# Optimization experiments

Measured on AMD Instinct MI355X. Metric: run time of the kernel, lower is better.

The kernel has to match this reference:

```python
import jax, jax.numpy as jnp
import numpy as np

N = 131072  # time steps
D = 4       # SDE state dimension


def setup_inputs() -> dict:
    key = jax.random.key(0)
    k = jax.random.split(key, 6)
    F = 0.1 * jax.random.normal(k[0], (D, D), jnp.float32)  # only shape/dtype used by filter
    H = jnp.zeros((1, D), jnp.float32).at[0, 0].set(1.0)    # observe first state component
    P_inf = jnp.eye(D, dtype=jnp.float32)
    # stable per-step transitions: spectral radius ~0.9
    A_seq = 0.9 * jnp.eye(D, dtype=jnp.float32)[None] + 0.02 * jax.random.normal(k[1], (N, D, D), jnp.float32)
    # PSD process noise per step
    S = 0.05 * jax.random.normal(k[2], (N, D, D), jnp.float32)
    Q_seq = jnp.einsum('nij,nkj->nik', S, S) + 1e-3 * jnp.eye(D, dtype=jnp.float32)[None]
    residual = jax.random.normal(k[3], (N,), jnp.float32)   # y - mean_fn(times)
    mask = jnp.ones((N,), jnp.float32)                      # all steps observed
    R_seq = 0.1 + 0.05 * jax.random.uniform(k[4], (N,), jnp.float32)  # noise_var + floor
    return dict(F=F, H=H, P_inf=P_inf, A_seq=A_seq, Q_seq=Q_seq,
                residual=residual, mask=mask, R_seq=R_seq)


def _kalman_filter(F, H, P_inf, A_seq, Q_seq, residual, mask, R_seq):
    d = F.shape[0]
    eye = jnp.eye(d, dtype=F.dtype)
    h = H[0]  # (d,)
    log_2pi = jnp.log(2.0 * jnp.pi).astype(F.dtype)

    def step(carry, inputs):
        m, P = carry
        A, Q, r_n, mask_n, R_n = inputs
        m_pred = A @ m
        P_pred = A @ P @ A.T + Q
        P_pred = 0.5 * (P_pred + P_pred.T)
        Ph = P_pred @ h                 # (d,)
        S = h @ Ph + R_n                # innovation variance
        innov = r_n - h @ m_pred
        is_obs = mask_n == 1
        S_safe = jnp.where(is_obs, S, 1.0)
        K = jnp.where(is_obs, Ph / S_safe, jnp.zeros_like(Ph))
        m_new = m_pred + K * innov
        I_KH = eye - K[:, None] * h[None, :]
        P_new = I_KH @ P_pred @ I_KH.T + R_n * (K[:, None] * K[None, :])
        P_new = 0.5 * (P_new + P_new.T)
        ll = jnp.where(is_obs, -0.5 * (log_2pi + jnp.log(S_safe) + innov * innov / S_safe), 0.0)
        return (m_new, P_new), (m_pred, P_pred, m_new, P_new, ll)

    m0 = jnp.zeros(d, dtype=F.dtype)
    _, (m_pred_seq, P_pred_seq, m_filt_seq, P_filt_seq, ll_seq) = jax.lax.scan(
        step, (m0, P_inf), (A_seq, Q_seq, residual, mask, R_seq))
    return m_pred_seq, P_pred_seq, m_filt_seq, P_filt_seq, jnp.sum(ll_seq)


def _rts_smoother(m_pred_seq, P_pred_seq, m_filt_seq, P_filt_seq, A_seq):
    def step(carry, inputs):
        m_ns, P_ns = carry
        m_f, P_f, m_pn, P_pn, A_n = inputs
        J = jnp.linalg.solve(P_pn.T, A_n @ P_f.T).T
        m_s = m_f + J @ (m_ns - m_pn)
        P_s = P_f + J @ (P_ns - P_pn) @ J.T
        P_s = 0.5 * (P_s + P_s.T)
        return (m_s, P_s), (m_s, P_s)

    m_T = m_filt_seq[-1]
    P_T = P_filt_seq[-1]
    inputs = (m_filt_seq[:-1], P_filt_seq[:-1], m_pred_seq[1:], P_pred_seq[1:], A_seq[1:])
    _, (m_s, P_s) = jax.lax.scan(step, (m_T, P_T), inputs, reverse=True)
    return (jnp.concatenate([m_s, m_T[None]], axis=0),
            jnp.concatenate([P_s, P_T[None]], axis=0))


def reference(F, H, P_inf, A_seq, Q_seq, residual, mask, R_seq):
    m_pred, P_pred, m_filt, P_filt, log_marginal = _kalman_filter(
        F, H, P_inf, A_seq, Q_seq, residual, mask, R_seq)
    m_smooth, P_smooth = _rts_smoother(m_pred, P_pred, m_filt, P_filt, A_seq)
    h = H[0]
    means = m_smooth @ h                                   # (N,) observation-space means
    vars_ = jnp.einsum('i,nij,j->n', h, P_smooth, h)       # (N,) marginal variances
    return means, vars_, log_marginal
```

## Files before the change

kernel.cpp:

```cpp
#include <hip/hip_runtime.h>
#include <math.h>

#define NN 131072
#define WUP 48
#define TPB 256
#define NBLK (NN / TPB)
#define WINF (TPB + WUP + 1)
#define WINB (TPB + WUP - 1)
#define LOG2PI 1.8378770664093453f

typedef __attribute__((ext_vector_type(2))) float f2;

__device__ float4 g_f[5][NN];
__device__ float4 g_J[4][NN];
__device__ float4 g_W[4][NN];
__device__ float4 g_u[NN];
__device__ double g_llb[NBLK];

__device__ __forceinline__ f2 bc(float s) {
  f2 r = {s, s};
  return r;
}
#define PF(a, b, c) __builtin_elementwise_fma((a), (b), (c))

template <int E>
__device__ __forceinline__ void ldpk(const float4 (*s)[E], int w, f2* M) {
#pragma unroll
  for (int c = 0; c < 4; ++c) {
    float4 v = s[c][w];
    M[2 * c] = f2{v.x, v.y};
    M[2 * c + 1] = f2{v.z, v.w};
  }
}

__device__ __forceinline__ void kf_step_pk(const f2* __restrict__ AT, const f2* __restrict__ Q,
                                           float r, float mk, float R, f2* __restrict__ m,
                                           f2* __restrict__ P, float& Ss, float& innov,
                                           bool& obs) {
  float m0 = m[0][0], m1 = m[0][1], m2_ = m[1][0], m3 = m[1][1];
  f2 mp[2];
#pragma unroll
  for (int p = 0; p < 2; ++p) {
    f2 acc = AT[p] * bc(m0);
    acc = PF(bc(m1), AT[2 + p], acc);
    acc = PF(bc(m2_), AT[4 + p], acc);
    acc = PF(bc(m3), AT[6 + p], acc);
    mp[p] = acc;
  }

  f2 T[8];
#pragma unroll
  for (int i = 0; i < 4; ++i) {
    float a0 = AT[0 + (i >> 1)][i & 1];
    float a1 = AT[2 + (i >> 1)][i & 1];
    float a2 = AT[4 + (i >> 1)][i & 1];
    float a3 = AT[6 + (i >> 1)][i & 1];
#pragma unroll
    for (int p = 0; p < 2; ++p) {
      f2 acc = P[p] * bc(a0);
      acc = PF(bc(a1), P[2 + p], acc);
      acc = PF(bc(a2), P[4 + p], acc);
      acc = PF(bc(a3), P[6 + p], acc);
      T[2 * i + p] = acc;
    }
  }

  f2 Pp[8];
#pragma unroll
  for (int i = 0; i < 4; ++i) {
    float t0 = T[2 * i][0], t1 = T[2 * i][1], t2 = T[2 * i + 1][0], t3 = T[2 * i + 1][1];
#pragma unroll
    for (int p = 0; p < 2; ++p) {
      f2 acc = PF(bc(t0), AT[p], Q[2 * i + p]);
      acc = PF(bc(t1), AT[2 + p], acc);
      acc = PF(bc(t2), AT[4 + p], acc);
      acc = PF(bc(t3), AT[6 + p], acc);
      Pp[2 * i + p] = acc;
    }
  }

  float S = Pp[0][0] + R;
  innov = r - mp[0][0];
  obs = (mk == 1.0f);
  Ss = obs ? S : 1.0f;
  float kf = obs ? (1.0f / Ss) : 0.0f;
  f2 K[2] = {Pp[0] * bc(kf), Pp[1] * bc(kf)};
#pragma unroll
  for (int p = 0; p < 2; ++p) m[p] = PF(K[p], bc(innov), mp[p]);

#pragma unroll
  for (int i = 0; i < 4; ++i) {
    float Ki = K[i >> 1][i & 1];
#pragma unroll
    for (int p = 0; p < 2; ++p) P[2 * i + p] = PF(bc(-Ki), Pp[p], Pp[2 * i + p]);
  }
}

__device__ __forceinline__ void chol_solve_pk(const f2* __restrict__ S, const f2* __restrict__ T,
                                              f2* __restrict__ X) {
  float s00 = S[0][0];
  float s10 = S[2][0], s11 = S[2][1];
  float s20 = S[4][0], s21 = S[4][1], s22 = S[5][0];
  float s30 = S[6][0], s31 = S[6][1], s32 = S[7][0], s33 = S[7][1];
  float l00 = sqrtf(s00), i00 = 1.f / l00;
  float l10 = s10 * i00, l20 = s20 * i00, l30 = s30 * i00;
  float l11 = sqrtf(s11 - l10 * l10), i11 = 1.f / l11;
  float l21 = (s21 - l20 * l10) * i11;
  float l31 = (s31 - l30 * l10) * i11;
  float l22 = sqrtf(s22 - l20 * l20 - l21 * l21), i22 = 1.f / l22;
  float l32 = (s32 - l30 * l20 - l31 * l21) * i22;
  float l33 = sqrtf(s33 - l30 * l30 - l31 * l31 - l32 * l32), i33 = 1.f / l33;
#pragma unroll
  for (int c = 0; c < 4; ++c) {
    float t0 = T[0 + (c >> 1)][c & 1];
    float t1 = T[2 + (c >> 1)][c & 1];
    float t2 = T[4 + (c >> 1)][c & 1];
    float t3 = T[6 + (c >> 1)][c & 1];
    float y0 = t0 * i00;
    float y1 = (t1 - l10 * y0) * i11;
    float y2 = (t2 - l20 * y0 - l21 * y1) * i22;
    float y3 = (t3 - l30 * y0 - l31 * y1 - l32 * y2) * i33;
    float x3 = y3 * i33;
    float x2 = (y2 - l32 * x3) * i22;
    float x1 = (y1 - l21 * x2 - l31 * x3) * i11;
    float x0 = (y0 - l10 * x1 - l20 * x2 - l30 * x3) * i00;
    X[0 + (c >> 1)][c & 1] = x0;
    X[2 + (c >> 1)][c & 1] = x1;
    X[4 + (c >> 1)][c & 1] = x2;
    X[6 + (c >> 1)][c & 1] = x3;
  }
}

__device__ __forceinline__ void make_record_pk(int n, const f2* __restrict__ m,
                                               const f2* __restrict__ P,
                                               const f2* __restrict__ AT,
                                               const f2* __restrict__ Q) {
  float m0 = m[0][0], m1 = m[0][1], m2_ = m[1][0], m3 = m[1][1];
  f2 pm[2];
#pragma unroll
  for (int p = 0; p < 2; ++p) {
    f2 acc = AT[p] * bc(m0);
    acc = PF(bc(m1), AT[2 + p], acc);
    acc = PF(bc(m2_), AT[4 + p], acc);
    acc = PF(bc(m3), AT[6 + p], acc);
    pm[p] = acc;
  }

  f2 T[8];
#pragma unroll
  for (int i = 0; i < 4; ++i) {
    float a0 = AT[0 + (i >> 1)][i & 1];
    float a1 = AT[2 + (i >> 1)][i & 1];
    float a2 = AT[4 + (i >> 1)][i & 1];
    float a3 = AT[6 + (i >> 1)][i & 1];
#pragma unroll
    for (int p = 0; p < 2; ++p) {
      f2 acc = P[p] * bc(a0);
      acc = PF(bc(a1), P[2 + p], acc);
      acc = PF(bc(a2), P[4 + p], acc);
      acc = PF(bc(a3), P[6 + p], acc);
      T[2 * i + p] = acc;
    }
  }

  f2 Ppn[8];
#pragma unroll
  for (int i = 0; i < 4; ++i) {
    float t0 = T[2 * i][0], t1 = T[2 * i][1], t2 = T[2 * i + 1][0], t3 = T[2 * i + 1][1];
#pragma unroll
    for (int p = 0; p < 2; ++p) {
      f2 acc = PF(bc(t0), AT[p], Q[2 * i + p]);
      acc = PF(bc(t1), AT[2 + p], acc);
      acc = PF(bc(t2), AT[4 + p], acc);
      acc = PF(bc(t3), AT[6 + p], acc);
      Ppn[2 * i + p] = acc;
    }
  }

  f2 X[8];
  chol_solve_pk(Ppn, T, X);

  float p0 = pm[0][0], p1 = pm[0][1], p2 = pm[1][0], p3 = pm[1][1];
  f2 u[2];
#pragma unroll
  for (int p = 0; p < 2; ++p) {
    f2 acc = X[p] * bc(p0);
    acc = PF(bc(p1), X[2 + p], acc);
    acc = PF(bc(p2), X[4 + p], acc);
    acc = PF(bc(p3), X[6 + p], acc);
    u[p] = m[p] - acc;
  }

  f2 Jp[8];
#pragma unroll
  for (int i = 0; i < 4; ++i) {
    float x0 = X[0 + (i >> 1)][i & 1];
    float x1 = X[2 + (i >> 1)][i & 1];
    float x2 = X[4 + (i >> 1)][i & 1];
    float x3 = X[6 + (i >> 1)][i & 1];
#pragma unroll
    for (int p = 0; p < 2; ++p) {
      f2 acc = Ppn[p] * bc(x0);
      acc = PF(bc(x1), Ppn[2 + p], acc);
      acc = PF(bc(x2), Ppn[4 + p], acc);
      acc = PF(bc(x3), Ppn[6 + p], acc);
      Jp[2 * i + p] = acc;
    }
  }
  f2 W[8];
#pragma unroll
  for (int i = 0; i < 4; ++i) {
    float j0 = Jp[2 * i][0], j1 = Jp[2 * i][1], j2 = Jp[2 * i + 1][0], j3 = Jp[2 * i + 1][1];
#pragma unroll
    for (int p = 0; p < 2; ++p) {
      f2 acc = X[p] * bc(j0);
      acc = PF(bc(j1), X[2 + p], acc);
      acc = PF(bc(j2), X[4 + p], acc);
      acc = PF(bc(j3), X[6 + p], acc);
      W[2 * i + p] = P[2 * i + p] - acc;
    }
  }

#pragma unroll
  for (int i = 0; i < 4; ++i)
    g_J[i][n] = make_float4(X[2 * i][0], X[2 * i][1], X[2 * i + 1][0], X[2 * i + 1][1]);
#pragma unroll
  for (int i = 0; i < 4; ++i)
    g_W[i][n] = make_float4(W[2 * i][0], W[2 * i][1], W[2 * i + 1][0], W[2 * i + 1][1]);
  g_u[n] = make_float4(u[0][0], u[0][1], u[1][0], u[1][1]);
}

__device__ __forceinline__ void rts_affine_pk(const f2* __restrict__ X, const f2* __restrict__ W,
                                              const f2* __restrict__ u, f2* __restrict__ ms,
                                              f2* __restrict__ Ps) {
  float s0 = ms[0][0], s1 = ms[0][1], s2 = ms[1][0], s3 = ms[1][1];
  f2 nms[2];
#pragma unroll
  for (int p = 0; p < 2; ++p) {
    f2 acc = PF(bc(s0), X[p], u[p]);
    acc = PF(bc(s1), X[2 + p], acc);
    acc = PF(bc(s2), X[4 + p], acc);
    acc = PF(bc(s3), X[6 + p], acc);
    nms[p] = acc;
  }
  f2 V[8];
#pragma unroll
  for (int i = 0; i < 4; ++i) {
    float x0 = X[0 + (i >> 1)][i & 1];
    float x1 = X[2 + (i >> 1)][i & 1];
    float x2 = X[4 + (i >> 1)][i & 1];
    float x3 = X[6 + (i >> 1)][i & 1];
#pragma unroll
    for (int p = 0; p < 2; ++p) {
      f2 acc = Ps[p] * bc(x0);
      acc = PF(bc(x1), Ps[2 + p], acc);
      acc = PF(bc(x2), Ps[4 + p], acc);
      acc = PF(bc(x3), Ps[6 + p], acc);
      V[2 * i + p] = acc;
    }
  }
#pragma unroll
  for (int i = 0; i < 4; ++i) {
    float v0 = V[2 * i][0], v1 = V[2 * i][1], v2 = V[2 * i + 1][0], v3 = V[2 * i + 1][1];
#pragma unroll
    for (int p = 0; p < 2; ++p) {
      f2 acc = PF(bc(v0), X[p], W[2 * i + p]);
      acc = PF(bc(v1), X[2 + p], acc);
      acc = PF(bc(v2), X[4 + p], acc);
      acc = PF(bc(v3), X[6 + p], acc);
      Ps[2 * i + p] = acc;
    }
  }
  ms[0] = nms[0];
  ms[1] = nms[1];
}

__global__ __launch_bounds__(TPB, 1) void fwd_kernel(const float* __restrict__ P_inf,
                                                     const float* __restrict__ A_seq,
                                                     const float* __restrict__ Q_seq,
                                                     const float* __restrict__ residual,
                                                     const float* __restrict__ mask,
                                                     const float* __restrict__ R_seq) {
  __shared__ float4 sAT[4][WINF], sQ[4][WINF];
  __shared__ float sr[WINF], smk[WINF], sR[WINF];
  __shared__ double sh[TPB];

  const int B = blockIdx.x * TPB;
  const int base = B - WUP;
  const float4* Af4 = (const float4*)A_seq;
  const float4* Qf4 = (const float4*)Q_seq;
  for (int f = threadIdx.x; f < WINF * 4; f += TPB) {
    int w = f >> 2, c = f & 3;
    int k = base + w;
    k = k < 0 ? 0 : (k > NN - 1 ? NN - 1 : k);
    float4 row = Af4[(size_t)k * 4 + c];
    ((float*)&sAT[0][w])[c] = row.x;
    ((float*)&sAT[1][w])[c] = row.y;
    ((float*)&sAT[2][w])[c] = row.z;
    ((float*)&sAT[3][w])[c] = row.w;
    sQ[c][w] = Qf4[(size_t)k * 4 + c];
  }
  for (int w = threadIdx.x; w < WINF; w += TPB) {
    int k = base + w;
    k = k < 0 ? 0 : (k > NN - 1 ? NN - 1 : k);
    sr[w] = residual[k];
    smk[w] = mask[k];
    sR[w] = R_seq[k];
  }
  __syncthreads();

  const int t = threadIdx.x;
  const int n = B + t;
  int s0 = n - WUP;
  if (s0 < 0) s0 = 0;

  f2 m[2] = {f2{0.f, 0.f}, f2{0.f, 0.f}};
  f2 P[8];
#pragma unroll
  for (int i = 0; i < 4; ++i) {
    P[2 * i] = f2{P_inf[i * 4 + 0], P_inf[i * 4 + 1]};
    P[2 * i + 1] = f2{P_inf[i * 4 + 2], P_inf[i * 4 + 3]};
  }

  float Ss = 1.f, innov = 0.f;
  bool obs = false;
  for (int k = s0; k <= n; ++k) {
    int w = k - base;
    f2 AT[8], Q[8];
    ldpk<WINF>(sAT, w, AT);
    ldpk<WINF>(sQ, w, Q);
    kf_step_pk(AT, Q, sr[w], smk[w], sR[w], m, P, Ss, innov, obs);
  }

#pragma unroll
  for (int c = 0; c < 4; ++c)
    g_f[c][n] = make_float4(P[2 * c][0], P[2 * c][1], P[2 * c + 1][0], P[2 * c + 1][1]);
  g_f[4][n] = make_float4(m[0][0], m[0][1], m[1][0], m[1][1]);

  if (n < NN - 1) {
    int w = n + 1 - base;
    f2 AT[8], Q[8];
    ldpk<WINF>(sAT, w, AT);
    ldpk<WINF>(sQ, w, Q);
    make_record_pk(n, m, P, AT, Q);
  }

  sh[t] = obs ? (double)(-0.5f * (LOG2PI + logf(Ss) + innov * innov / Ss)) : 0.0;
  __syncthreads();
#pragma unroll
  for (int w = TPB / 2; w > 0; w >>= 1) {
    if (t < w) sh[t] += sh[t + w];
    __syncthreads();
  }
  if (t == 0) g_llb[blockIdx.x] = sh[0];
}

__global__ __launch_bounds__(TPB, 1) void bwd_kernel(float* __restrict__ out) {
  __shared__ float4 sX[4][WINB], sW[4][WINB];
  __shared__ float4 su[WINB];
  __shared__ double shd[TPB];

  const int B = blockIdx.x * TPB;
  const int t = threadIdx.x;
  const int n = B + t;
  int e = n + WUP;
  if (e > NN - 1) e = NN - 1;

  f2 ms[2], Ps[8];
#pragma unroll
  for (int c = 0; c < 4; ++c) {
    float4 v = g_f[c][e];
    Ps[2 * c] = f2{v.x, v.y};
    Ps[2 * c + 1] = f2{v.z, v.w};
  }
  {
    float4 v = g_f[4][e];
    ms[0] = f2{v.x, v.y};
    ms[1] = f2{v.z, v.w};
  }

  for (int f = t; f < WINB * 4; f += TPB) {
    int w = f >> 2, c = f & 3;
    int k = B + w;
    if (k > NN - 1) k = NN - 1;
    sX[c][w] = g_J[c][k];
    sW[c][w] = g_W[c][k];
  }
  for (int w = t; w < WINB; w += TPB) {
    int k = B + w;
    if (k > NN - 1) k = NN - 1;
    su[w] = g_u[k];
  }
  __syncthreads();

  for (int k = e - 1; k >= n; --k) {
    int w = k - B;
    f2 X[8], W[8];
    ldpk<WINB>(sX, w, X);
    ldpk<WINB>(sW, w, W);
    float4 v = su[w];
    f2 u[2] = {f2{v.x, v.y}, f2{v.z, v.w}};
    rts_affine_pk(X, W, u, ms, Ps);
  }

  out[n] = ms[0][0];
  out[NN + n] = Ps[0][0];

  if (blockIdx.x == 0) {
    double acc = 0.0;
    for (int i = t; i < NBLK; i += TPB) acc += g_llb[i];
    shd[t] = acc;
    __syncthreads();
#pragma unroll
    for (int w = TPB / 2; w > 0; w >>= 1) {
      if (t < w) shd[t] += shd[t + w];
      __syncthreads();
    }
    if (t == 0) out[2 * NN] = (float)shd[0];
  }
}

extern "C" void kernel_launch(void* const* d_in, const int* in_sizes, int n_in, void* d_out,
                              int out_size, void* d_ws, size_t ws_size, hipStream_t stream) {
  const float* P_inf = (const float*)d_in[2];
  const float* A_seq = (const float*)d_in[3];
  const float* Q_seq = (const float*)d_in[4];
  const float* residual = (const float*)d_in[5];
  const float* mask = (const float*)d_in[6];
  const float* R_seq = (const float*)d_in[7];
  float* out = (float*)d_out;

  fwd_kernel<<<NBLK, TPB, 0, stream>>>(P_inf, A_seq, Q_seq, residual, mask, R_seq);
  bwd_kernel<<<NBLK, TPB, 0, stream>>>(out);
}
```

Before: 136.1 us.

## Store symmetric Q and W matrices as packed upper triangles and shrink warm-up window

Q in shared memory and the RTS W term in global and shared memory are now stored as 10-float upper triangles instead of full 4x4 matrices, then expanded to full rows in registers. This cuts shared-memory reads in the sequential inner loops and global traffic between the forward and backward kernels. The warm-up length also drops from 48 to 40 steps, which shortens every thread's redundant prefix recompute but gives the windowed filter and smoother less distance to converge, so accuracy may suffer. W is assumed symmetric; if it is not exactly symmetric, the packed form changes results slightly.

```diff
diff --git a/kernel.cpp b/kernel.cpp
--- a/kernel.cpp
+++ b/kernel.cpp
@@ -2,7 +2,7 @@
 #include <math.h>
 
 #define NN 131072
-#define WUP 48
+#define WUP 40
 #define TPB 256
 #define NBLK (NN / TPB)
 #define WINF (TPB + WUP + 1)
@@ -13,7 +13,9 @@
 
 __device__ float4 g_f[5][NN];
 __device__ float4 g_J[4][NN];
-__device__ float4 g_W[4][NN];
+__device__ float4 g_W0[NN];
+__device__ float4 g_W1[NN];
+__device__ float2 g_W2[NN];
 __device__ float4 g_u[NN];
 __device__ double g_llb[NBLK];
 
@@ -31,6 +33,18 @@
     M[2 * c] = f2{v.x, v.y};
     M[2 * c + 1] = f2{v.z, v.w};
   }
+}
+
+__device__ __forceinline__ void sym_rows(const float4 t0, const float4 t1, const float2 t2,
+                                         f2* M) {
+  M[0] = f2{t0.x, t0.y};
+  M[1] = f2{t0.z, t0.w};
+  M[2] = f2{t0.y, t1.x};
+  M[3] = f2{t1.y, t1.z};
+  M[4] = f2{t0.z, t1.y};
+  M[5] = f2{t1.w, t2.x};
+  M[6] = f2{t0.w, t1.z};
+  M[7] = f2{t2.x, t2.y};
 }
 
 __device__ __forceinline__ void kf_step_pk(const f2* __restrict__ AT, const f2* __restrict__ Q,
@@ -224,9 +238,9 @@
 #pragma unroll
   for (int i = 0; i < 4; ++i)
     g_J[i][n] = make_float4(X[2 * i][0], X[2 * i][1], X[2 * i + 1][0], X[2 * i + 1][1]);
-#pragma unroll
-  for (int i = 0; i < 4; ++i)
-    g_W[i][n] = make_float4(W[2 * i][0], W[2 * i][1], W[2 * i + 1][0], W[2 * i + 1][1]);
+  g_W0[n] = make_float4(W[0][0], W[0][1], W[1][0], W[1][1]);
+  g_W1[n] = make_float4(W[2][1], W[3][0], W[3][1], W[5][0]);
+  g_W2[n] = make_float2(W[5][1], W[7][1]);
   g_u[n] = make_float4(u[0][0], u[0][1], u[1][0], u[1][1]);
 }
 
@@ -281,7 +295,9 @@
                                                      const float* __restrict__ residual,
                                                      const float* __restrict__ mask,
                                                      const float* __restrict__ R_seq) {
-  __shared__ float4 sAT[4][WINF], sQ[4][WINF];
+  __shared__ float4 sAT[4][WINF];
+  __shared__ float4 sQ0[WINF], sQ1[WINF];
+  __shared__ float2 sQ2[WINF];
   __shared__ float sr[WINF], smk[WINF], sR[WINF];
   __shared__ double sh[TPB];
 
@@ -293,12 +309,24 @@
     int w = f >> 2, c = f & 3;
     int k = base + w;
     k = k < 0 ? 0 : (k > NN - 1 ? NN - 1 : k);
-    float4 row = Af4[(size_t)k * 4 + c];
-    ((float*)&sAT[0][w])[c] = row.x;
-    ((float*)&sAT[1][w])[c] = row.y;
-    ((float*)&sAT[2][w])[c] = row.z;
-    ((float*)&sAT[3][w])[c] = row.w;
-    sQ[c][w] = Qf4[(size_t)k * 4 + c];
+    float4 rowA = Af4[(size_t)k * 4 + c];
+    ((float*)&sAT[0][w])[c] = rowA.x;
+    ((float*)&sAT[1][w])[c] = rowA.y;
+    ((float*)&sAT[2][w])[c] = rowA.z;
+    ((float*)&sAT[3][w])[c] = rowA.w;
+    float4 rowQ = Qf4[(size_t)k * 4 + c];
+    if (c == 0) {
+      sQ0[w] = rowQ;
+    } else if (c == 1) {
+      sQ1[w].x = rowQ.y;
+      sQ1[w].y = rowQ.z;
+      sQ1[w].z = rowQ.w;
+    } else if (c == 2) {
+      sQ1[w].w = rowQ.z;
+      sQ2[w].x = rowQ.w;
+    } else {
+      sQ2[w].y = rowQ.w;
+    }
   }
   for (int w = threadIdx.x; w < WINF; w += TPB) {
     int k = base + w;
@@ -328,7 +356,7 @@
     int w = k - base;
     f2 AT[8], Q[8];
     ldpk<WINF>(sAT, w, AT);
-    ldpk<WINF>(sQ, w, Q);
+    sym_rows(sQ0[w], sQ1[w], sQ2[w], Q);
     kf_step_pk(AT, Q, sr[w], smk[w], sR[w], m, P, Ss, innov, obs);
   }
 
@@ -341,7 +369,7 @@
     int w = n + 1 - base;
     f2 AT[8], Q[8];
     ldpk<WINF>(sAT, w, AT);
-    ldpk<WINF>(sQ, w, Q);
+    sym_rows(sQ0[w], sQ1[w], sQ2[w], Q);
     make_record_pk(n, m, P, AT, Q);
   }
 
@@ -356,7 +384,9 @@
 }
 
 __global__ __launch_bounds__(TPB, 1) void bwd_kernel(float* __restrict__ out) {
-  __shared__ float4 sX[4][WINB], sW[4][WINB];
+  __shared__ float4 sX[4][WINB];
+  __shared__ float4 sW0[WINB], sW1[WINB];
+  __shared__ float2 sW2[WINB];
   __shared__ float4 su[WINB];
   __shared__ double shd[TPB];
 
@@ -384,11 +414,13 @@
     int k = B + w;
     if (k > NN - 1) k = NN - 1;
     sX[c][w] = g_J[c][k];
-    sW[c][w] = g_W[c][k];
   }
   for (int w = t; w < WINB; w += TPB) {
     int k = B + w;
     if (k > NN - 1) k = NN - 1;
+    sW0[w] = g_W0[k];
+    sW1[w] = g_W1[k];
+    sW2[w] = g_W2[k];
     su[w] = g_u[k];
   }
   __syncthreads();
@@ -397,7 +429,7 @@
     int w = k - B;
     f2 X[8], W[8];
     ldpk<WINB>(sX, w, X);
-    ldpk<WINB>(sW, w, W);
+    sym_rows(sW0[w], sW1[w], sW2[w], W);
     float4 v = su[w];
     f2 u[2] = {f2{v.x, v.y}, f2{v.z, v.w}};
     rts_affine_pk(X, W, u, ms, Ps);
```

New measurement: 132.6 us. 1.03x faster.
